# Performance work log

Measured on AMD Instinct MI355X. Metric: run time of the kernel, lower is better.

The kernel has to match this reference:

```python
import jax, jax.numpy as jnp
import numpy as np

NUM_CATEGORIES = 32
INPUT_DIM = 1024
HIDDEN_DIM = 4096
BATCH = 64
SEQ = 512


def setup_inputs() -> dict:
    key = jax.random.key(0)
    k_x, k_w, k_c = jax.random.split(key, 3)
    x = jax.random.normal(k_x, (BATCH, SEQ, INPUT_DIM), dtype=jnp.float32)
    W = 0.02 * jax.random.normal(k_w, (NUM_CATEGORIES, INPUT_DIM, HIDDEN_DIM), dtype=jnp.float32)
    b = jnp.zeros((NUM_CATEGORIES, HIDDEN_DIM), dtype=jnp.float32)
    cat_ids = jax.random.randint(k_c, (BATCH,), 0, NUM_CATEGORIES, dtype=jnp.int64)
    return {"x": x, "cat_ids": cat_ids, "W": W, "b": b}


def reference(x, cat_ids, W, b):
    # Gather per-sample weight/bias by category, then batched matmul.
    selected_W = W[cat_ids]              # [B, input_dim, hidden_dim]
    selected_b = b[cat_ids]              # [B, hidden_dim]
    out = jnp.einsum('bsi,bih->bsh', x, selected_W)  # [B, S, hidden_dim]
    return out + selected_b[:, None, :]
```

## Files before the change

### kernel.cpp

```cpp
#include <hip/hip_runtime.h>
#include <stdint.h>

#define B_ 64
#define S_ 512
#define K_ 1024
#define H_ 4096
#define C_ 32

typedef float  f32x4  __attribute__((ext_vector_type(4)));
typedef short  bf16x8 __attribute__((ext_vector_type(8)));
typedef unsigned short u16x8 __attribute__((ext_vector_type(8)));
typedef __attribute__((address_space(3))) unsigned int as3u32;
typedef const __attribute__((address_space(1))) unsigned int as1u32;

__device__ __forceinline__ unsigned short f2bf(float f) {
    unsigned u = __builtin_bit_cast(unsigned, f);
    u += 0x7fffu + ((u >> 16) & 1u);
    return (unsigned short)(u >> 16);
}

__global__ void fix_cat_kernel(const void* __restrict__ cat_raw, int* __restrict__ cat32) {
    int t = threadIdx.x;
    const long long* c64 = (const long long*)cat_raw;
    const int*       c32 = (const int*)cat_raw;
    long long v = (t < 32) ? c64[t] : 0;
    int bad = (t < 32) && (v < 0 || v >= C_);
    unsigned long long m = __ballot(bad);
    if (m == 0ULL) {
        cat32[t] = (int)c64[t];
    } else {
        cat32[t] = c32[t];
    }
}

__global__ __launch_bounds__(256) void cvt_x_kernel(const float4* __restrict__ x,
                                                    uint4* __restrict__ xb, int n8) {
    int stride = gridDim.x * blockDim.x;
    for (int i = blockIdx.x * blockDim.x + threadIdx.x; i < n8; i += stride) {
        float4 a = x[2 * i], b = x[2 * i + 1];
        uint4 o;
        o.x = (unsigned)f2bf(a.x) | ((unsigned)f2bf(a.y) << 16);
        o.y = (unsigned)f2bf(a.z) | ((unsigned)f2bf(a.w) << 16);
        o.z = (unsigned)f2bf(b.x) | ((unsigned)f2bf(b.y) << 16);
        o.w = (unsigned)f2bf(b.z) | ((unsigned)f2bf(b.w) << 16);
        xb[i] = o;
    }
}

__global__ __launch_bounds__(256) void cvt_w_kernel(const float* __restrict__ W,
                                                    unsigned short* __restrict__ WT) {
    __shared__ unsigned short tile[64 * 68];
    const int nt = blockIdx.x;
    const int kt = blockIdx.y;
    const int c  = blockIdx.z;
    const int t  = threadIdx.x;

    const float* Wp = W + ((size_t)c << 22);
#pragma unroll
    for (int p = 0; p < 4; ++p) {
        int task = p * 256 + t;
        int kr = task >> 4;
        int nc = (task & 15) << 2;
        float4 v = *(const float4*)(Wp + (size_t)(kt * 64 + kr) * H_ + nt * 64 + nc);
        tile[kr * 68 + nc + 0] = f2bf(v.x);
        tile[kr * 68 + nc + 1] = f2bf(v.y);
        tile[kr * 68 + nc + 2] = f2bf(v.z);
        tile[kr * 68 + nc + 3] = f2bf(v.w);
    }
    __syncthreads();

    unsigned short* WTp = WT + ((size_t)c << 22);
#pragma unroll
    for (int q = 0; q < 2; ++q) {
        int task = q * 256 + t;
        int nl = task >> 3;
        int ko = (task & 7) << 3;
        u16x8 o;
#pragma unroll
        for (int j = 0; j < 8; ++j) o[j] = tile[(ko + j) * 68 + nl];
        *(u16x8*)(WTp + (size_t)(nt * 64 + nl) * K_ + kt * 64 + ko) = o;
    }
}

__global__ __launch_bounds__(512, 2) void gemm2_kernel(
    const unsigned short* __restrict__ xb,
    const unsigned short* __restrict__ WT,
    const float* __restrict__ bias,
    const int* __restrict__ cat,
    float* __restrict__ out)
{
    extern __shared__ __align__(16) char smem[];

    const int t    = threadIdx.x;
    const int lane = t & 63;
    const int w    = t >> 6;
    const int wm   = w >> 2;
    const int wn   = w & 3;
    const int lo   = lane & 15;
    const int hi   = lane >> 4;

    const int wg = (blockIdx.x & 7) * 256 + (blockIdx.x >> 3);
    const int bn = wg & 15;
    const int bm = (wg >> 4) & 1;
    const int bb = wg >> 5;

    const int c = cat[bb];

    const unsigned short* Ap = xb + (size_t)bb * (S_ * K_) + (size_t)(bm * 256) * K_;
    const unsigned short* Bp = WT + (size_t)c * ((size_t)H_ * K_) + (size_t)(bn * 256) * K_;

    const int srow  = lane >> 2;
    const int sslot = (lane & 3) ^ hi;
    const char* srcA[2]; const char* srcB[2];
    int offA[2], offB[2];
#pragma unroll
    for (int i = 0; i < 2; ++i) {
        int ch = i * 8 + w;
        int r  = ch * 16 + srow;
        srcA[i] = (const char*)(Ap + (size_t)r * K_ + sslot * 8);
        srcB[i] = (const char*)(Bp + (size_t)r * K_ + sslot * 8);
        offA[i] = ch * 1024;
        offB[i] = 16384 + ch * 1024;
    }

    const int xslot = (hi ^ ((lo >> 2) & 3)) << 4;
    int aoff[8], boff[4];
#pragma unroll
    for (int mi = 0; mi < 8; ++mi) aoff[mi] = (wm * 128 + mi * 16 + lo) * 64 + xslot;
#pragma unroll
    for (int ni = 0; ni < 4; ++ni) boff[ni] = 16384 + (wn * 64 + ni * 16 + lo) * 64 + xslot;

    f32x4 acc[8][4];
#pragma unroll
    for (int mi = 0; mi < 8; ++mi)
#pragma unroll
        for (int ni = 0; ni < 4; ++ni) acc[mi][ni] = f32x4{0.f, 0.f, 0.f, 0.f};

#define STAGE(s_, d_) do {                                                        \
    const int s__ = (s_);                                                         \
    char* dst__ = smem + (d_) * 32768;                                            \
    __builtin_amdgcn_global_load_lds((as1u32*)(srcA[0] + s__ * 64),               \
                                     (as3u32*)(dst__ + offA[0]), 16, 0, 0);       \
    __builtin_amdgcn_global_load_lds((as1u32*)(srcB[0] + s__ * 64),               \
                                     (as3u32*)(dst__ + offB[0]), 16, 0, 0);       \
    __builtin_amdgcn_global_load_lds((as1u32*)(srcA[1] + s__ * 64),               \
                                     (as3u32*)(dst__ + offA[1]), 16, 0, 0);       \
    __builtin_amdgcn_global_load_lds((as1u32*)(srcB[1] + s__ * 64),               \
                                     (as3u32*)(dst__ + offB[1]), 16, 0, 0);       \
} while (0)

    STAGE(0, 0); STAGE(1, 1); STAGE(2, 2);

#pragma unroll 4
    for (int tt = 0; tt < 32; ++tt) {
        asm volatile("s_waitcnt vmcnt(8)" ::: "memory");
        __builtin_amdgcn_s_barrier();
        asm volatile("" ::: "memory");

        STAGE((tt + 3) & 31, (tt + 3) & 3);

        const char* buf = smem + (tt & 3) * 32768;
        bf16x8 av[8], bv[4];
#pragma unroll
        for (int mi = 0; mi < 8; ++mi) av[mi] = *(const bf16x8*)(buf + aoff[mi]);
#pragma unroll
        for (int ni = 0; ni < 4; ++ni) bv[ni] = *(const bf16x8*)(buf + boff[ni]);

        __builtin_amdgcn_s_setprio(1);
#pragma unroll
        for (int mi = 0; mi < 8; ++mi)
#pragma unroll
            for (int ni = 0; ni < 4; ++ni)
                acc[mi][ni] = __builtin_amdgcn_mfma_f32_16x16x32_bf16(
                    bv[ni], av[mi], acc[mi][ni], 0, 0, 0);
        __builtin_amdgcn_s_setprio(0);
    }
#undef STAGE

    asm volatile("s_waitcnt vmcnt(0)" ::: "memory");

    float* outp = out + ((size_t)bb * S_ + bm * 256 + wm * 128) * H_ + bn * 256 + wn * 64;
    const float* bp = bias + (size_t)c * H_ + bn * 256 + wn * 64;
#pragma unroll
    for (int ni = 0; ni < 4; ++ni) {
        const int nf = ni * 16 + hi * 4;
        const f32x4 b4 = *(const f32x4*)(bp + nf);
#pragma unroll
        for (int mi = 0; mi < 8; ++mi) {
            const int mf = mi * 16 + lo;
            f32x4 v = acc[mi][ni];
            v.x += b4.x; v.y += b4.y; v.z += b4.z; v.w += b4.w;
            *(f32x4*)(outp + (size_t)mf * H_ + nf) = v;
        }
    }
}

__global__ __launch_bounds__(256) void fallback_kernel(
    const float* __restrict__ x, const int* __restrict__ cat,
    const float* __restrict__ W, const float* __restrict__ bias,
    float* __restrict__ out)
{
    __shared__ float xs[K_];
    int bs = blockIdx.x;
    int bb = bs >> 9;
    int c  = cat[bb];
    const float* xp = x + (size_t)bs * K_;
    for (int i = threadIdx.x; i < K_ / 4; i += 256)
        ((float4*)xs)[i] = ((const float4*)xp)[i];
    __syncthreads();

    int h = blockIdx.y * 1024 + threadIdx.x * 4;
    const float* Wp = W + (size_t)c * K_ * H_ + h;
    float a0 = 0.f, a1 = 0.f, a2 = 0.f, a3 = 0.f;
    for (int k = 0; k < K_; ++k) {
        float xv = xs[k];
        float4 wv = *(const float4*)(Wp + (size_t)k * H_);
        a0 += xv * wv.x; a1 += xv * wv.y; a2 += xv * wv.z; a3 += xv * wv.w;
    }
    float4 bv = *(const float4*)(bias + c * H_ + h);
    float4 o; o.x = a0 + bv.x; o.y = a1 + bv.y; o.z = a2 + bv.z; o.w = a3 + bv.w;
    *(float4*)(out + (size_t)bs * H_ + h) = o;
}

extern "C" void kernel_launch(void* const* d_in, const int* in_sizes, int n_in,
                              void* d_out, int out_size, void* d_ws, size_t ws_size,
                              hipStream_t stream) {
    const float* x        = (const float*)d_in[0];
    const void*  cat_raw  = d_in[1];
    const float* W        = (const float*)d_in[2];
    const float* bias     = (const float*)d_in[3];
    float*       out      = (float*)d_out;

    const size_t CAT_BYTES = 256;
    const size_t XB_OFF    = 256;
    const size_t XB_BYTES  = (size_t)B_ * S_ * K_ * 2;
    const size_t WT_OFF    = XB_OFF + XB_BYTES;
    const size_t WT_BYTES  = (size_t)C_ * H_ * K_ * 2;
    const size_t NEED      = WT_OFF + WT_BYTES;

    const int* catp;
    if (ws_size >= CAT_BYTES) {
        int* cat32 = (int*)d_ws;
        fix_cat_kernel<<<1, 64, 0, stream>>>(cat_raw, cat32);
        catp = cat32;
    } else {
        catp = (const int*)cat_raw;
    }

    if (ws_size >= NEED) {
        unsigned short* xb = (unsigned short*)((char*)d_ws + XB_OFF);
        unsigned short* WT = (unsigned short*)((char*)d_ws + WT_OFF);
        cvt_x_kernel<<<2048, 256, 0, stream>>>((const float4*)x, (uint4*)xb,
                                               (int)((size_t)B_ * S_ * K_ / 8));
        dim3 gw(64, 16, 32);
        cvt_w_kernel<<<gw, 256, 0, stream>>>(W, WT);
        hipFuncSetAttribute((const void*)gemm2_kernel,
                            hipFuncAttributeMaxDynamicSharedMemorySize, 131072);
        gemm2_kernel<<<2048, 512, 131072, stream>>>(xb, WT, bias, catp, out);
    } else {
        dim3 g(B_ * S_, H_ / 1024);
        fallback_kernel<<<g, 256, 0, stream>>>(x, catp, W, bias, out);
    }
}
```

Measured before the change: 566.2 us.

## Split each k-step into two phases interleaving LDS reads, staging, and MFMAs

Each main-loop iteration now runs in two halves. The A-tile global-to-LDS stage is issued after the first half of the LDS fragment reads, and the B-tile stage after the second, with barriers and sched_barriers between them. The aim is to spread global load issue across the MFMA work and keep LDS reads, DMA and matrix ops interleaved in a ping-pong schedule. In exchange it adds two extra barriers per iteration plus explicit lgkmcnt waits, which could add synchronisation stalls.

```diff
diff --git a/kernel.cpp b/kernel.cpp
--- a/kernel.cpp
+++ b/kernel.cpp
@@ -136,46 +136,74 @@
 #pragma unroll
         for (int ni = 0; ni < 4; ++ni) acc[mi][ni] = f32x4{0.f, 0.f, 0.f, 0.f};
 
-#define STAGE(s_, d_) do {                                                        \
-    const int s__ = (s_);                                                         \
-    char* dst__ = smem + (d_) * 32768;                                            \
-    __builtin_amdgcn_global_load_lds((as1u32*)(srcA[0] + s__ * 64),               \
-                                     (as3u32*)(dst__ + offA[0]), 16, 0, 0);       \
-    __builtin_amdgcn_global_load_lds((as1u32*)(srcB[0] + s__ * 64),               \
-                                     (as3u32*)(dst__ + offB[0]), 16, 0, 0);       \
-    __builtin_amdgcn_global_load_lds((as1u32*)(srcA[1] + s__ * 64),               \
-                                     (as3u32*)(dst__ + offA[1]), 16, 0, 0);       \
-    __builtin_amdgcn_global_load_lds((as1u32*)(srcB[1] + s__ * 64),               \
-                                     (as3u32*)(dst__ + offB[1]), 16, 0, 0);       \
+#define STAGE_A(s_, d_) do {                                                      \
+    const int sa__ = (s_);                                                        \
+    char* da__ = smem + (d_) * 32768;                                             \
+    __builtin_amdgcn_global_load_lds((as1u32*)(srcA[0] + sa__ * 64),              \
+                                     (as3u32*)(da__ + offA[0]), 16, 0, 0);        \
+    __builtin_amdgcn_global_load_lds((as1u32*)(srcA[1] + sa__ * 64),              \
+                                     (as3u32*)(da__ + offA[1]), 16, 0, 0);        \
 } while (0)
-
-    STAGE(0, 0); STAGE(1, 1); STAGE(2, 2);
+#define STAGE_B(s_, d_) do {                                                      \
+    const int sb__ = (s_);                                                        \
+    char* db__ = smem + (d_) * 32768;                                             \
+    __builtin_amdgcn_global_load_lds((as1u32*)(srcB[0] + sb__ * 64),              \
+                                     (as3u32*)(db__ + offB[0]), 16, 0, 0);        \
+    __builtin_amdgcn_global_load_lds((as1u32*)(srcB[1] + sb__ * 64),              \
+                                     (as3u32*)(db__ + offB[1]), 16, 0, 0);        \
+} while (0)
+
+    STAGE_A(0, 0); STAGE_B(0, 0);
+    STAGE_A(1, 1); STAGE_B(1, 1);
+    STAGE_A(2, 2); STAGE_B(2, 2);
+    asm volatile("s_waitcnt vmcnt(8)" ::: "memory");
+    __builtin_amdgcn_s_barrier();
 
 #pragma unroll 4
     for (int tt = 0; tt < 32; ++tt) {
-        asm volatile("s_waitcnt vmcnt(8)" ::: "memory");
-        __builtin_amdgcn_s_barrier();
+        const char* buf = smem + (tt & 3) * 32768;
+        const int sN = (tt + 3) & 31, dN = (tt + 3) & 3;
+        bf16x8 av[4], bv[4], aw[4];
+
+#pragma unroll
+        for (int mi = 0; mi < 4; ++mi) av[mi] = *(const bf16x8*)(buf + aoff[mi]);
+#pragma unroll
+        for (int ni = 0; ni < 4; ++ni) bv[ni] = *(const bf16x8*)(buf + boff[ni]);
+        STAGE_A(sN, dN);
         asm volatile("" ::: "memory");
-
-        STAGE((tt + 3) & 31, (tt + 3) & 3);
-
-        const char* buf = smem + (tt & 3) * 32768;
-        bf16x8 av[8], bv[4];
-#pragma unroll
-        for (int mi = 0; mi < 8; ++mi) av[mi] = *(const bf16x8*)(buf + aoff[mi]);
-#pragma unroll
-        for (int ni = 0; ni < 4; ++ni) bv[ni] = *(const bf16x8*)(buf + boff[ni]);
-
+        __builtin_amdgcn_s_barrier();
+        asm volatile("s_waitcnt lgkmcnt(0)" ::: "memory");
+        __builtin_amdgcn_sched_barrier(0);
         __builtin_amdgcn_s_setprio(1);
 #pragma unroll
-        for (int mi = 0; mi < 8; ++mi)
+        for (int mi = 0; mi < 4; ++mi)
 #pragma unroll
             for (int ni = 0; ni < 4; ++ni)
                 acc[mi][ni] = __builtin_amdgcn_mfma_f32_16x16x32_bf16(
                     bv[ni], av[mi], acc[mi][ni], 0, 0, 0);
         __builtin_amdgcn_s_setprio(0);
-    }
-#undef STAGE
+        __builtin_amdgcn_s_barrier();
+
+#pragma unroll
+        for (int mi = 0; mi < 4; ++mi) aw[mi] = *(const bf16x8*)(buf + aoff[mi + 4]);
+        STAGE_B(sN, dN);
+        asm volatile("" ::: "memory");
+        __builtin_amdgcn_s_barrier();
+        asm volatile("s_waitcnt lgkmcnt(0)" ::: "memory");
+        __builtin_amdgcn_sched_barrier(0);
+        __builtin_amdgcn_s_setprio(1);
+#pragma unroll
+        for (int mi = 0; mi < 4; ++mi)
+#pragma unroll
+            for (int ni = 0; ni < 4; ++ni)
+                acc[mi + 4][ni] = __builtin_amdgcn_mfma_f32_16x16x32_bf16(
+                    bv[ni], aw[mi], acc[mi + 4][ni], 0, 0, 0);
+        __builtin_amdgcn_s_setprio(0);
+        asm volatile("s_waitcnt vmcnt(8)" ::: "memory");
+        __builtin_amdgcn_s_barrier();
+    }
+#undef STAGE_A
+#undef STAGE_B
 
     asm volatile("s_waitcnt vmcnt(0)" ::: "memory");
 
```

New measurement: 567.1 us. About the same (+0.2%).

## Switch GEMM to 32x32x16 MFMA with triple-buffered split-phase LDS pipeline

Applied to the files above, without the earlier changes.

Replaces the 16x16x32 bf16 MFMA tiling with 32x32x16 MFMAs on f32x16 accumulators. This cuts the number of LDS fragment reads per k-step and raises math per instruction. The LDS ring drops from 4 stages to 3 rotating buffers (96KB). Each 64-wide k-tile is split into two halves, with the next half's LDS reads and the A/B global loads interleaved against MFMAs using explicit lgkmcnt/vmcnt waits and sched barriers. Output stores become nontemporal. The risks are tighter wait counts and a changed swizzle, which could stall or cause bank conflicts.

```diff
diff --git a/kernel.cpp b/kernel.cpp
--- a/kernel.cpp
+++ b/kernel.cpp
@@ -7,8 +7,9 @@
 #define H_ 4096
 #define C_ 32
 
-typedef float  f32x4  __attribute__((ext_vector_type(4)));
-typedef short  bf16x8 __attribute__((ext_vector_type(8)));
+typedef float  f32x4   __attribute__((ext_vector_type(4)));
+typedef float  f32x16  __attribute__((ext_vector_type(16)));
+typedef short  bf16x8  __attribute__((ext_vector_type(8)));
 typedef unsigned short u16x8 __attribute__((ext_vector_type(8)));
 typedef __attribute__((address_space(3))) unsigned int as3u32;
 typedef const __attribute__((address_space(1))) unsigned int as1u32;
@@ -82,7 +83,7 @@
     }
 }
 
-__global__ __launch_bounds__(512, 2) void gemm2_kernel(
+__global__ __launch_bounds__(512, 2) void gemm5_kernel(
     const unsigned short* __restrict__ xb,
     const unsigned short* __restrict__ WT,
     const float* __restrict__ bias,
@@ -96,8 +97,9 @@
     const int w    = t >> 6;
     const int wm   = w >> 2;
     const int wn   = w & 3;
-    const int lo   = lane & 15;
-    const int hi   = lane >> 4;
+    const int l31  = lane & 31;
+    const int hi2  = lane >> 5;
+    const int x2   = (l31 >> 1) & 3;
 
     const int wg = (blockIdx.x & 7) * 256 + (blockIdx.x >> 3);
     const int bn = wg & 15;
@@ -110,87 +112,116 @@
     const unsigned short* Bp = WT + (size_t)c * ((size_t)H_ * K_) + (size_t)(bn * 256) * K_;
 
     const int srow  = lane >> 2;
-    const int sslot = (lane & 3) ^ hi;
-    const char* srcA[2]; const char* srcB[2];
-    int offA[2], offB[2];
-#pragma unroll
-    for (int i = 0; i < 2; ++i) {
-        int ch = i * 8 + w;
-        int r  = ch * 16 + srow;
-        srcA[i] = (const char*)(Ap + (size_t)r * K_ + sslot * 8);
-        srcB[i] = (const char*)(Bp + (size_t)r * K_ + sslot * 8);
-        offA[i] = ch * 1024;
-        offB[i] = 16384 + ch * 1024;
-    }
-
-    const int xslot = (hi ^ ((lo >> 2) & 3)) << 4;
-    int aoff[8], boff[4];
-#pragma unroll
-    for (int mi = 0; mi < 8; ++mi) aoff[mi] = (wm * 128 + mi * 16 + lo) * 64 + xslot;
-#pragma unroll
-    for (int ni = 0; ni < 4; ++ni) boff[ni] = 16384 + (wn * 64 + ni * 16 + lo) * 64 + xslot;
-
-    f32x4 acc[8][4];
-#pragma unroll
-    for (int mi = 0; mi < 8; ++mi)
-#pragma unroll
-        for (int ni = 0; ni < 4; ++ni) acc[mi][ni] = f32x4{0.f, 0.f, 0.f, 0.f};
-
-#define STAGE(s_, d_) do {                                                        \
-    const int s__ = (s_);                                                         \
-    char* dst__ = smem + (d_) * 32768;                                            \
-    __builtin_amdgcn_global_load_lds((as1u32*)(srcA[0] + s__ * 64),               \
-                                     (as3u32*)(dst__ + offA[0]), 16, 0, 0);       \
-    __builtin_amdgcn_global_load_lds((as1u32*)(srcB[0] + s__ * 64),               \
-                                     (as3u32*)(dst__ + offB[0]), 16, 0, 0);       \
-    __builtin_amdgcn_global_load_lds((as1u32*)(srcA[1] + s__ * 64),               \
-                                     (as3u32*)(dst__ + offA[1]), 16, 0, 0);       \
-    __builtin_amdgcn_global_load_lds((as1u32*)(srcB[1] + s__ * 64),               \
-                                     (as3u32*)(dst__ + offB[1]), 16, 0, 0);       \
+    const int sslot = (lane & 3) ^ ((lane >> 3) & 3);
+    const char* sA0 = (const char*)(Ap + (size_t)((0 * 8 + w) * 16 + srow) * K_) + sslot * 16;
+    const char* sA1 = (const char*)(Ap + (size_t)((1 * 8 + w) * 16 + srow) * K_) + sslot * 16;
+    const char* sB0 = (const char*)(Bp + (size_t)((0 * 8 + w) * 16 + srow) * K_) + sslot * 16;
+    const char* sB1 = (const char*)(Bp + (size_t)((1 * 8 + w) * 16 + srow) * K_) + sslot * 16;
+    const int dc0 = (0 * 8 + w) * 1024;
+    const int dc1 = (1 * 8 + w) * 1024;
+
+    int aB[4], bB[2];
+#pragma unroll
+    for (int mi = 0; mi < 4; ++mi) aB[mi] = (wm * 128 + mi * 32 + l31) * 64;
+#pragma unroll
+    for (int ni = 0; ni < 2; ++ni) bB[ni] = 16384 + (wn * 64 + ni * 32 + l31) * 64;
+    const int so0 = ((0 * 2 + hi2) ^ x2) << 4;
+    const int so1 = ((1 * 2 + hi2) ^ x2) << 4;
+
+    f32x16 acc[4][2];
+#pragma unroll
+    for (int mi = 0; mi < 4; ++mi)
+#pragma unroll
+        for (int ni = 0; ni < 2; ++ni)
+#pragma unroll
+            for (int e = 0; e < 16; ++e) acc[mi][ni][e] = 0.f;
+
+#define GLD(src_, dst_) __builtin_amdgcn_global_load_lds((as1u32*)(src_), (as3u32*)(dst_), 16, 0, 0)
+#define SA(tl_, sp_) do { const int o_ = (tl_) * 64;                              \
+    GLD(sA0 + o_, (sp_) + dc0); GLD(sA1 + o_, (sp_) + dc1); } while (0)
+#define SB(tl_, sp_) do { const int o_ = (tl_) * 64;                              \
+    GLD(sB0 + o_, (sp_) + 16384 + dc0); GLD(sB1 + o_, (sp_) + 16384 + dc1); } while (0)
+#define RD6(p_, so_, ra_, rb_) do {                                               \
+    ra_[0] = *(const bf16x8*)((p_) + aB[0] + (so_));                              \
+    ra_[1] = *(const bf16x8*)((p_) + aB[1] + (so_));                              \
+    ra_[2] = *(const bf16x8*)((p_) + aB[2] + (so_));                              \
+    ra_[3] = *(const bf16x8*)((p_) + aB[3] + (so_));                              \
+    rb_[0] = *(const bf16x8*)((p_) + bB[0] + (so_));                              \
+    rb_[1] = *(const bf16x8*)((p_) + bB[1] + (so_));                              \
 } while (0)
-
-    STAGE(0, 0); STAGE(1, 1); STAGE(2, 2);
-
-#pragma unroll 4
-    for (int tt = 0; tt < 32; ++tt) {
-        asm volatile("s_waitcnt vmcnt(8)" ::: "memory");
+#define MFMA8(ra_, rb_) do {                                                      \
+    _Pragma("unroll")                                                             \
+    for (int mi = 0; mi < 4; ++mi)                                                \
+        _Pragma("unroll")                                                         \
+        for (int ni = 0; ni < 2; ++ni)                                            \
+            acc[mi][ni] = __builtin_amdgcn_mfma_f32_32x32x16_bf16(                \
+                rb_[ni], ra_[mi], acc[mi][ni], 0, 0, 0);                          \
+} while (0)
+
+    char* p0 = smem;
+    char* p1 = smem + 32768;
+    char* p2 = smem + 65536;
+
+    SA(0, p0); SB(0, p0);
+    SA(1, p1); SB(1, p1);
+    asm volatile("s_waitcnt vmcnt(4)" ::: "memory");
+    __builtin_amdgcn_s_barrier();
+
+    bf16x8 pa[4], pb[2], qa[4], qb[2];
+    RD6(p0, so0, pa, pb);
+
+#pragma unroll 1
+    for (int T = 0; T < 32; ++T) {
+        const int tl2 = (T + 2) & 31;
+
+        RD6(p0, so1, qa, qb);
+        SA(tl2, p2);
+        asm volatile("s_waitcnt lgkmcnt(6)" ::: "memory");
+        __builtin_amdgcn_sched_barrier(0);
+        __builtin_amdgcn_s_setprio(1);
+        MFMA8(pa, pb);
+        __builtin_amdgcn_s_setprio(0);
+
+        asm volatile("s_waitcnt lgkmcnt(0)" ::: "memory");
+        __builtin_amdgcn_sched_barrier(0);
+        asm volatile("s_waitcnt vmcnt(2)" ::: "memory");
         __builtin_amdgcn_s_barrier();
-        asm volatile("" ::: "memory");
-
-        STAGE((tt + 3) & 31, (tt + 3) & 3);
-
-        const char* buf = smem + (tt & 3) * 32768;
-        bf16x8 av[8], bv[4];
-#pragma unroll
-        for (int mi = 0; mi < 8; ++mi) av[mi] = *(const bf16x8*)(buf + aoff[mi]);
-#pragma unroll
-        for (int ni = 0; ni < 4; ++ni) bv[ni] = *(const bf16x8*)(buf + boff[ni]);
-
+        RD6(p1, so0, pa, pb);
+        SB(tl2, p2);
+        asm volatile("s_waitcnt lgkmcnt(6)" ::: "memory");
+        __builtin_amdgcn_sched_barrier(0);
         __builtin_amdgcn_s_setprio(1);
-#pragma unroll
-        for (int mi = 0; mi < 8; ++mi)
-#pragma unroll
-            for (int ni = 0; ni < 4; ++ni)
-                acc[mi][ni] = __builtin_amdgcn_mfma_f32_16x16x32_bf16(
-                    bv[ni], av[mi], acc[mi][ni], 0, 0, 0);
+        MFMA8(qa, qb);
         __builtin_amdgcn_s_setprio(0);
-    }
-#undef STAGE
-
-    asm volatile("s_waitcnt vmcnt(0)" ::: "memory");
+
+        char* tmp = p0; p0 = p1; p1 = p2; p2 = tmp;
+    }
+#undef MFMA8
+#undef RD6
+#undef SB
+#undef SA
+#undef GLD
+
+    asm volatile("s_waitcnt vmcnt(0) lgkmcnt(0)" ::: "memory");
 
     float* outp = out + ((size_t)bb * S_ + bm * 256 + wm * 128) * H_ + bn * 256 + wn * 64;
     const float* bp = bias + (size_t)c * H_ + bn * 256 + wn * 64;
 #pragma unroll
-    for (int ni = 0; ni < 4; ++ni) {
-        const int nf = ni * 16 + hi * 4;
-        const f32x4 b4 = *(const f32x4*)(bp + nf);
-#pragma unroll
-        for (int mi = 0; mi < 8; ++mi) {
-            const int mf = mi * 16 + lo;
-            f32x4 v = acc[mi][ni];
-            v.x += b4.x; v.y += b4.y; v.z += b4.z; v.w += b4.w;
-            *(f32x4*)(outp + (size_t)mf * H_ + nf) = v;
+    for (int mi = 0; mi < 4; ++mi) {
+        float* orow = outp + (size_t)(mi * 32 + l31) * H_;
+#pragma unroll
+        for (int ni = 0; ni < 2; ++ni) {
+#pragma unroll
+            for (int g = 0; g < 4; ++g) {
+                const int nf = ni * 32 + 8 * g + 4 * hi2;
+                const f32x4 b4 = *(const f32x4*)(bp + nf);
+                f32x4 v;
+                v.x = acc[mi][ni][4 * g + 0] + b4.x;
+                v.y = acc[mi][ni][4 * g + 1] + b4.y;
+                v.z = acc[mi][ni][4 * g + 2] + b4.z;
+                v.w = acc[mi][ni][4 * g + 3] + b4.w;
+                __builtin_nontemporal_store(v, (f32x4*)(orow + nf));
+            }
         }
     }
 }
@@ -254,9 +285,9 @@
                                                (int)((size_t)B_ * S_ * K_ / 8));
         dim3 gw(64, 16, 32);
         cvt_w_kernel<<<gw, 256, 0, stream>>>(W, WT);
-        hipFuncSetAttribute((const void*)gemm2_kernel,
-                            hipFuncAttributeMaxDynamicSharedMemorySize, 131072);
-        gemm2_kernel<<<2048, 512, 131072, stream>>>(xb, WT, bias, catp, out);
+        hipFuncSetAttribute((const void*)gemm5_kernel,
+                            hipFuncAttributeMaxDynamicSharedMemorySize, 98304);
+        gemm5_kernel<<<2048, 512, 98304, stream>>>(xb, WT, bias, catp, out);
     } else {
         dim3 g(B_ * S_, H_ / 1024);
         fallback_kernel<<<g, 256, 0, stream>>>(x, catp, W, bias, out);
```

Result: slower. 751.1 us (+32.7%).
